# Kernel tuning notes

Hardware: AMD Instinct MI355X
Metric: run time of the kernel (lower is better)

Reference implementation:

```python
import jax, jax.numpy as jnp
import numpy as np

HEADS = 64
VOCAB = 5
EPS = 1e-5

def _layer_norm(x, g, b):
    mu = jnp.mean(x, axis=-1, keepdims=True)
    var = jnp.var(x, axis=-1, keepdims=True)
    return (x - mu) * jax.lax.rsqrt(var + EPS) * g + b

def setup_inputs() -> dict:
    key = jax.random.key(0)
    ks = jax.random.split(key, 12)
    h = HEADS
    s = 1.0 / np.sqrt(h)
    return {
        "x": jax.random.normal(ks[0], (8, 384, 384, h), dtype=jnp.float32),
        "W1": jax.random.normal(ks[1], (h, h), dtype=jnp.float32) * s,
        "b1": jnp.zeros((h,), jnp.float32),
        "W2": jax.random.normal(ks[2], (h, h), dtype=jnp.float32) * s,
        "b2": jnp.zeros((h,), jnp.float32),
        "W3": jax.random.normal(ks[3], (h, h), dtype=jnp.float32) * s,
        "b3": jnp.zeros((h,), jnp.float32),
        "ln_g": jnp.ones((h,), jnp.float32),
        "ln_b": jnp.zeros((h,), jnp.float32),
        "Wo": jax.random.normal(ks[4], (h, VOCAB), dtype=jnp.float32) * s,
        "bo": jnp.zeros((VOCAB,), jnp.float32),
    }

def reference(x, W1, b1, W2, b2, W3, b3, ln_g, ln_b, Wo, bo):
    # three (Linear -> gelu -> shared LayerNorm) blocks on [b,s,s,h]
    h = _layer_norm(jax.nn.gelu(x @ W1 + b1, approximate=False), ln_g, ln_b)
    h = _layer_norm(jax.nn.gelu(h @ W2 + b2, approximate=False), ln_g, ln_b)
    h = _layer_norm(jax.nn.gelu(h @ W3 + b3, approximate=False), ln_g, ln_b)
    out = h @ Wo + bo  # [b,s,s,vocab]
    return (out + jnp.swapaxes(out, 1, 2)) * 0.5
```

## Files before the change

### kernel.cpp

```cpp
#include <hip/hip_runtime.h>
#include <cstdint>
#include <cstddef>

typedef __attribute__((ext_vector_type(8))) __bf16   bf16x8;
typedef __attribute__((ext_vector_type(2))) __bf16   bf16x2;
typedef __attribute__((ext_vector_type(4))) float    f32x4;
typedef __attribute__((ext_vector_type(4))) uint32_t u32x4;

#define SDIM     384
#define VOCAB    5
#define SPW      8
#define WGPB     288
#define BLOCKS   (8 * WGPB)

#define WO_OFF   24576
#define BIAS_OFF 26624
#define OUT_OFF  27392

__device__ __forceinline__ f32x4 gelu4(f32x4 x){
  f32x4 u = x * x;
  f32x4 w = u * (-0.10294456f) + (-2.3021255f);
  f32x4 z = x * w;
  f32x4 e;
  e[0] = __builtin_amdgcn_exp2f(z[0]);
  e[1] = __builtin_amdgcn_exp2f(z[1]);
  e[2] = __builtin_amdgcn_exp2f(z[2]);
  e[3] = __builtin_amdgcn_exp2f(z[3]);
  f32x4 d = e + 1.0f;
  f32x4 r;
  r[0] = __builtin_amdgcn_rcpf(d[0]);
  r[1] = __builtin_amdgcn_rcpf(d[1]);
  r[2] = __builtin_amdgcn_rcpf(d[2]);
  r[3] = __builtin_amdgcn_rcpf(d[3]);
  return x * r;
}

__device__ __forceinline__ bf16x8 mk_bf8(f32x4 a, f32x4 b){
  bf16x8 v;
  v[0]=(__bf16)a[0]; v[1]=(__bf16)a[1]; v[2]=(__bf16)a[2]; v[3]=(__bf16)a[3];
  v[4]=(__bf16)b[0]; v[5]=(__bf16)b[1]; v[6]=(__bf16)b[2]; v[7]=(__bf16)b[3];
  return v;
}

__device__ __forceinline__ int perm_rho(int m){
  return (m & 0x23) | ((m & 4) << 2) | ((m & 0x18) >> 1);
}

__global__ __launch_bounds__(256)
void mlp_sym_kernel(const float* __restrict__ x,
                    const float* __restrict__ W1, const float* __restrict__ b1,
                    const float* __restrict__ W2, const float* __restrict__ b2,
                    const float* __restrict__ W3, const float* __restrict__ b3,
                    const float* __restrict__ lng, const float* __restrict__ lnb,
                    const float* __restrict__ Wo,  const float* __restrict__ bo,
                    float* __restrict__ out)
{
  __shared__ __align__(16) uint8_t Wl[37632];

  const int tid = threadIdx.x;

  {
    int m = tid & 63, g = tid >> 6;
    int rho = perm_rho(m);
    uint8_t* wrow = Wl + rho * 128;
    int swz = (rho & 7) << 4;
    #pragma unroll 1
    for (int idx = g; idx < 96; idx += 4) {
      int L = idx >> 5, kp = idx & 31;
      const float* W = (L == 0) ? W1 : ((L == 1) ? W2 : W3);
      float lo = W[(2 * kp    ) * 64 + m];
      float hi = W[(2 * kp + 1) * 64 + m];
      bf16x2 p = { (__bf16)lo, (__bf16)hi };
      *(uint32_t*)(wrow + L * 8192 + ((4 * kp) ^ swz)) = __builtin_bit_cast(uint32_t, p);
    }
    int mm = tid & 15;
    #pragma unroll 1
    for (int kp = tid >> 4; kp < 32; kp += 16) {
      float lo = (mm < VOCAB) ? Wo[(2 * kp    ) * VOCAB + mm] : 0.0f;
      float hi = (mm < VOCAB) ? Wo[(2 * kp + 1) * VOCAB + mm] : 0.0f;
      bf16x2 p = { (__bf16)lo, (__bf16)hi };
      *(uint32_t*)(Wl + WO_OFF + mm * 128 + ((4 * kp) ^ ((mm & 7) << 4))) =
          __builtin_bit_cast(uint32_t, p);
    }
    if (tid < 192) {
      float v = (tid < 64) ? b1[tid] : ((tid < 128) ? b2[tid - 64] : b3[tid - 128]);
      *(float*)(Wl + BIAS_OFF + tid * 4) = v;
    }
  }
  __syncthreads();

  const int bb  = blockIdx.x / WGPB;
  const int rem = blockIdx.x - bb * WGPB;
  int I0, J0, I1, J1;
  bool diag;
  if (rem < 276) {
    int I = 0, acc = 0;
    while (acc + (23 - I) <= rem) { acc += 23 - I; ++I; }
    int J = I + 1 + (rem - acc);
    I0 = I << 4; J0 = J << 4; I1 = J << 4; J1 = I << 4; diag = false;
  } else {
    int d = rem - 276;
    I0 = J0 = (2 * d) << 4; I1 = J1 = (2 * d + 1) << 4; diag = true;
  }

  const int wav  = tid >> 6, lane = tid & 63;
  const int h    = lane >> 4;
  const int b    = lane & 15;
  const int swzW = (b & 7) << 4;
  const int rowB = b * 128;
  const int kOff = 16 * h;
  const float* biasL = (const float*)(Wl + BIAS_OFF);
  float* outS = (float*)(Wl + OUT_OFF);

  const int blk  = wav >> 1, half = wav & 1;
  const int rowb = (blk ? I1 : I0) + 8 * half;
  const int colb = (blk ? J1 : J0);
  const long base0 = ((long)(bb * SDIM + rowb)) * SDIM + colb;

  f32x4 ggr[4], bbr[4], aoInit;
  #pragma unroll
  for (int mt = 0; mt < 4; ++mt) {
    int base = 8 * h + 4 * (mt & 1) + 32 * (mt >> 1);
    ggr[mt] = *(const f32x4*)(lng + base);
    bbr[mt] = *(const f32x4*)(lnb + base);
  }
  #pragma unroll
  for (int r = 0; r < 4; ++r) {
    int v = 4 * h + r;
    aoInit[r] = (v < VOCAB) ? bo[v] : 0.0f;
  }

  f32x4 xn[4];
  {
    const float* px = x + (size_t)(base0 + b) * 64 + 8 * h;
    xn[0] = *(const f32x4*)(px);      xn[1] = *(const f32x4*)(px + 4);
    xn[2] = *(const f32x4*)(px + 32); xn[3] = *(const f32x4*)(px + 36);
  }

  #pragma unroll 1
  for (int i = 0; i < SPW; ++i) {
    u32x4 bfr[2];
    bfr[0] = __builtin_bit_cast(u32x4, mk_bf8(xn[0], xn[1]));
    bfr[1] = __builtin_bit_cast(u32x4, mk_bf8(xn[2], xn[3]));

    {
      int inext = (i + 1 < SPW) ? (i + 1) : i;
      const float* pn = x + (size_t)(base0 + inext * SDIM + b) * 64 + 8 * h;
      xn[0] = *(const f32x4*)(pn);      xn[1] = *(const f32x4*)(pn + 4);
      xn[2] = *(const f32x4*)(pn + 32); xn[3] = *(const f32x4*)(pn + 36);
    }

    #pragma unroll
    for (int L = 0; L < 3; ++L) {
      const uint8_t* wp = Wl + L * 8192 + rowB;
      f32x4 acc[4];
      #pragma unroll
      for (int mt = 0; mt < 4; ++mt) {
        u32x4 w0 = *(const u32x4*)(wp + mt * 2048 + ((kOff     ) ^ swzW));
        u32x4 w1 = *(const u32x4*)(wp + mt * 2048 + ((kOff + 64) ^ swzW));
        int base = 8 * h + 4 * (mt & 1) + 32 * (mt >> 1);
        acc[mt] = *(const f32x4*)(biasL + L * 64 + base);
        acc[mt] = __builtin_amdgcn_mfma_f32_16x16x32_bf16(
            __builtin_bit_cast(bf16x8, w0), __builtin_bit_cast(bf16x8, bfr[0]), acc[mt], 0, 0, 0);
        acc[mt] = __builtin_amdgcn_mfma_f32_16x16x32_bf16(
            __builtin_bit_cast(bf16x8, w1), __builtin_bit_cast(bf16x8, bfr[1]), acc[mt], 0, 0, 0);
      }

      #pragma unroll
      for (int mt = 0; mt < 4; ++mt) acc[mt] = gelu4(acc[mt]);

      f32x4 vs = acc[0] + acc[1] + acc[2] + acc[3];
      f32x4 vq = acc[0]*acc[0] + acc[1]*acc[1] + acc[2]*acc[2] + acc[3]*acc[3];
      float s1 = (vs[0]+vs[1]) + (vs[2]+vs[3]);
      float s2 = (vq[0]+vq[1]) + (vq[2]+vq[3]);
      s1 += __shfl_xor(s1, 16); s2 += __shfl_xor(s2, 16);
      s1 += __shfl_xor(s1, 32); s2 += __shfl_xor(s2, 32);
      float mu   = s1 * (1.0f/64.0f);
      float var  = __builtin_fmaf(s2, (1.0f/64.0f), -mu * mu);
      float rstd = rsqrtf(var + 1e-5f);
      float nm   = -mu * rstd;

      f32x4 n0 = (acc[0] * rstd + nm) * ggr[0] + bbr[0];
      f32x4 n1 = (acc[1] * rstd + nm) * ggr[1] + bbr[1];
      f32x4 n2 = (acc[2] * rstd + nm) * ggr[2] + bbr[2];
      f32x4 n3 = (acc[3] * rstd + nm) * ggr[3] + bbr[3];
      bfr[0] = __builtin_bit_cast(u32x4, mk_bf8(n0, n1));
      bfr[1] = __builtin_bit_cast(u32x4, mk_bf8(n2, n3));
    }

    f32x4 ao = aoInit;
    {
      const uint8_t* wp = Wl + WO_OFF + rowB;
      u32x4 w0 = *(const u32x4*)(wp + ((kOff     ) ^ swzW));
      u32x4 w1 = *(const u32x4*)(wp + ((kOff + 64) ^ swzW));
      ao = __builtin_amdgcn_mfma_f32_16x16x32_bf16(
          __builtin_bit_cast(bf16x8, w0), __builtin_bit_cast(bf16x8, bfr[0]), ao, 0, 0, 0);
      ao = __builtin_amdgcn_mfma_f32_16x16x32_bf16(
          __builtin_bit_cast(bf16x8, w1), __builtin_bit_cast(bf16x8, bfr[1]), ao, 0, 0, 0);
    }

    float* myF = outS + blk * 1280 + (8 * half + i) * 80;
    #pragma unroll
    for (int r = 0; r < 4; ++r) {
      int v = 4 * h + r;
      if (v < VOCAB) myF[b * VOCAB + v] = ao[r];
    }
  }
  __syncthreads();

  #pragma unroll 1
  for (int idx = tid; idx < 2560; idx += 256) {
    int bk = (idx >= 1280) ? 1 : 0;
    int q2 = idx - bk * 1280;
    int r  = q2 / 80;
    int q  = q2 - r * 80;
    int c  = q / 5;
    int v  = q - c * 5;
    int pb = diag ? bk : 1 - bk;
    float val = 0.5f * (outS[bk * 1280 + r * 80 + q] +
                        outS[pb * 1280 + c * 80 + r * 5 + v]);
    int ii = (bk ? I1 : I0) + r;
    int jj = (bk ? J1 : J0) + c;
    out[((size_t)(bb * SDIM + ii) * SDIM + jj) * VOCAB + v] = val;
  }
}

extern "C" void kernel_launch(void* const* d_in, const int* in_sizes, int n_in,
                              void* d_out, int out_size, void* d_ws, size_t ws_size,
                              hipStream_t stream)
{
  const float* x   = (const float*)d_in[0];
  const float* W1  = (const float*)d_in[1];
  const float* b1  = (const float*)d_in[2];
  const float* W2  = (const float*)d_in[3];
  const float* b2  = (const float*)d_in[4];
  const float* W3  = (const float*)d_in[5];
  const float* b3  = (const float*)d_in[6];
  const float* lng = (const float*)d_in[7];
  const float* lnb = (const float*)d_in[8];
  const float* Wo  = (const float*)d_in[9];
  const float* bo  = (const float*)d_in[10];

  float* out = (float*)d_out;

  mlp_sym_kernel<<<BLOCKS, 256, 0, stream>>>(x, W1, b1, W2, b2, W3, b3,
                                             lng, lnb, Wo, bo, out);
}
```

Measured before the change: 136.8 us.

## Convert to persistent kernel with atomic work-stealing over tile units

The kernel now launches a fixed grid of 512 persistent blocks that fetch tile-pair units from a global atomic counter, instead of one block per unit. Weights are staged into LDS once per block rather than once per unit, and load balance is dynamic. The cost is an extra memset launch, an atomic per unit, and an extra barrier per unit. 512 blocks may also under-fill the device's CUs compared with the original 2304-block grid.

```diff
diff --git a/kernel.cpp b/kernel.cpp
--- a/kernel.cpp
+++ b/kernel.cpp
@@ -11,11 +11,13 @@
 #define VOCAB    5
 #define SPW      8
 #define WGPB     288
-#define BLOCKS   (8 * WGPB)
+#define UNITS    (8 * WGPB)
+#define PBLOCKS  512
 
 #define WO_OFF   24576
 #define BIAS_OFF 26624
 #define OUT_OFF  27392
+#define NU_OFF   37632
 
 __device__ __forceinline__ f32x4 gelu4(f32x4 x){
   f32x4 u = x * x;
@@ -46,53 +48,10 @@
   return (m & 0x23) | ((m & 4) << 2) | ((m & 0x18) >> 1);
 }
 
-__global__ __launch_bounds__(256)
-void mlp_sym_kernel(const float* __restrict__ x,
-                    const float* __restrict__ W1, const float* __restrict__ b1,
-                    const float* __restrict__ W2, const float* __restrict__ b2,
-                    const float* __restrict__ W3, const float* __restrict__ b3,
-                    const float* __restrict__ lng, const float* __restrict__ lnb,
-                    const float* __restrict__ Wo,  const float* __restrict__ bo,
-                    float* __restrict__ out)
-{
-  __shared__ __align__(16) uint8_t Wl[37632];
-
-  const int tid = threadIdx.x;
-
-  {
-    int m = tid & 63, g = tid >> 6;
-    int rho = perm_rho(m);
-    uint8_t* wrow = Wl + rho * 128;
-    int swz = (rho & 7) << 4;
-    #pragma unroll 1
-    for (int idx = g; idx < 96; idx += 4) {
-      int L = idx >> 5, kp = idx & 31;
-      const float* W = (L == 0) ? W1 : ((L == 1) ? W2 : W3);
-      float lo = W[(2 * kp    ) * 64 + m];
-      float hi = W[(2 * kp + 1) * 64 + m];
-      bf16x2 p = { (__bf16)lo, (__bf16)hi };
-      *(uint32_t*)(wrow + L * 8192 + ((4 * kp) ^ swz)) = __builtin_bit_cast(uint32_t, p);
-    }
-    int mm = tid & 15;
-    #pragma unroll 1
-    for (int kp = tid >> 4; kp < 32; kp += 16) {
-      float lo = (mm < VOCAB) ? Wo[(2 * kp    ) * VOCAB + mm] : 0.0f;
-      float hi = (mm < VOCAB) ? Wo[(2 * kp + 1) * VOCAB + mm] : 0.0f;
-      bf16x2 p = { (__bf16)lo, (__bf16)hi };
-      *(uint32_t*)(Wl + WO_OFF + mm * 128 + ((4 * kp) ^ ((mm & 7) << 4))) =
-          __builtin_bit_cast(uint32_t, p);
-    }
-    if (tid < 192) {
-      float v = (tid < 64) ? b1[tid] : ((tid < 128) ? b2[tid - 64] : b3[tid - 128]);
-      *(float*)(Wl + BIAS_OFF + tid * 4) = v;
-    }
-  }
-  __syncthreads();
-
-  const int bb  = blockIdx.x / WGPB;
-  const int rem = blockIdx.x - bb * WGPB;
-  int I0, J0, I1, J1;
-  bool diag;
+__device__ __forceinline__ void decode_unit(int u, int& bb, int& I0, int& J0,
+                                            int& I1, int& J1, bool& diag){
+  bb = u / WGPB;
+  int rem = u - bb * WGPB;
   if (rem < 276) {
     int I = 0, acc = 0;
     while (acc + (23 - I) <= rem) { acc += 23 - I; ++I; }
@@ -102,6 +61,50 @@
     int d = rem - 276;
     I0 = J0 = (2 * d) << 4; I1 = J1 = (2 * d + 1) << 4; diag = true;
   }
+}
+
+__global__ __launch_bounds__(256)
+void mlp_sym_kernel(const float* __restrict__ x,
+                    const float* __restrict__ W1, const float* __restrict__ b1,
+                    const float* __restrict__ W2, const float* __restrict__ b2,
+                    const float* __restrict__ W3, const float* __restrict__ b3,
+                    const float* __restrict__ lng, const float* __restrict__ lnb,
+                    const float* __restrict__ Wo,  const float* __restrict__ bo,
+                    float* __restrict__ out, unsigned int* __restrict__ counter)
+{
+  __shared__ __align__(16) uint8_t Wl[37696];
+
+  const int tid = threadIdx.x;
+
+  {
+    int m = tid & 63, g = tid >> 6;
+    int rho = perm_rho(m);
+    uint8_t* wrow = Wl + rho * 128;
+    int swz = (rho & 7) << 4;
+    #pragma unroll 1
+    for (int idx = g; idx < 96; idx += 4) {
+      int L = idx >> 5, kp = idx & 31;
+      const float* W = (L == 0) ? W1 : ((L == 1) ? W2 : W3);
+      float lo = W[(2 * kp    ) * 64 + m];
+      float hi = W[(2 * kp + 1) * 64 + m];
+      bf16x2 p = { (__bf16)lo, (__bf16)hi };
+      *(uint32_t*)(wrow + L * 8192 + ((4 * kp) ^ swz)) = __builtin_bit_cast(uint32_t, p);
+    }
+    int mm = tid & 15;
+    #pragma unroll 1
+    for (int kp = tid >> 4; kp < 32; kp += 16) {
+      float lo = (mm < VOCAB) ? Wo[(2 * kp    ) * VOCAB + mm] : 0.0f;
+      float hi = (mm < VOCAB) ? Wo[(2 * kp + 1) * VOCAB + mm] : 0.0f;
+      bf16x2 p = { (__bf16)lo, (__bf16)hi };
+      *(uint32_t*)(Wl + WO_OFF + mm * 128 + ((4 * kp) ^ ((mm & 7) << 4))) =
+          __builtin_bit_cast(uint32_t, p);
+    }
+    if (tid < 192) {
+      float v = (tid < 64) ? b1[tid] : ((tid < 128) ? b2[tid - 64] : b3[tid - 128]);
+      *(float*)(Wl + BIAS_OFF + tid * 4) = v;
+    }
+  }
+  __syncthreads();
 
   const int wav  = tid >> 6, lane = tid & 63;
   const int h    = lane >> 4;
@@ -111,11 +114,8 @@
   const int kOff = 16 * h;
   const float* biasL = (const float*)(Wl + BIAS_OFF);
   float* outS = (float*)(Wl + OUT_OFF);
-
+  volatile int* nuS = (volatile int*)(Wl + NU_OFF);
   const int blk  = wav >> 1, half = wav & 1;
-  const int rowb = (blk ? I1 : I0) + 8 * half;
-  const int colb = (blk ? J1 : J0);
-  const long base0 = ((long)(bb * SDIM + rowb)) * SDIM + colb;
 
   f32x4 ggr[4], bbr[4], aoInit;
   #pragma unroll
@@ -130,98 +130,115 @@
     aoInit[r] = (v < VOCAB) ? bo[v] : 0.0f;
   }
 
-  f32x4 xn[4];
-  {
-    const float* px = x + (size_t)(base0 + b) * 64 + 8 * h;
-    xn[0] = *(const f32x4*)(px);      xn[1] = *(const f32x4*)(px + 4);
-    xn[2] = *(const f32x4*)(px + 32); xn[3] = *(const f32x4*)(px + 36);
-  }
-
-  #pragma unroll 1
-  for (int i = 0; i < SPW; ++i) {
-    u32x4 bfr[2];
-    bfr[0] = __builtin_bit_cast(u32x4, mk_bf8(xn[0], xn[1]));
-    bfr[1] = __builtin_bit_cast(u32x4, mk_bf8(xn[2], xn[3]));
-
+  int u = blockIdx.x;
+
+  while (u < UNITS) {
+    int bb, I0, J0, I1, J1; bool diag;
+    decode_unit(u, bb, I0, J0, I1, J1, diag);
+
+    const int rowb = (blk ? I1 : I0) + 8 * half;
+    const int colb = (blk ? J1 : J0);
+    const long base0 = ((long)(bb * SDIM + rowb)) * SDIM + colb;
+
+    f32x4 xn[4];
     {
-      int inext = (i + 1 < SPW) ? (i + 1) : i;
-      const float* pn = x + (size_t)(base0 + inext * SDIM + b) * 64 + 8 * h;
-      xn[0] = *(const f32x4*)(pn);      xn[1] = *(const f32x4*)(pn + 4);
-      xn[2] = *(const f32x4*)(pn + 32); xn[3] = *(const f32x4*)(pn + 36);
-    }
-
-    #pragma unroll
-    for (int L = 0; L < 3; ++L) {
-      const uint8_t* wp = Wl + L * 8192 + rowB;
-      f32x4 acc[4];
+      const float* px = x + (size_t)(base0 + b) * 64 + 8 * h;
+      xn[0] = *(const f32x4*)(px);      xn[1] = *(const f32x4*)(px + 4);
+      xn[2] = *(const f32x4*)(px + 32); xn[3] = *(const f32x4*)(px + 36);
+    }
+
+    #pragma unroll 1
+    for (int i = 0; i < SPW; ++i) {
+      u32x4 bfr[2];
+      bfr[0] = __builtin_bit_cast(u32x4, mk_bf8(xn[0], xn[1]));
+      bfr[1] = __builtin_bit_cast(u32x4, mk_bf8(xn[2], xn[3]));
+
+      {
+        int inext = (i + 1 < SPW) ? (i + 1) : i;
+        const float* pn = x + (size_t)(base0 + inext * SDIM + b) * 64 + 8 * h;
+        xn[0] = *(const f32x4*)(pn);      xn[1] = *(const f32x4*)(pn + 4);
+        xn[2] = *(const f32x4*)(pn + 32); xn[3] = *(const f32x4*)(pn + 36);
+      }
+
       #pragma unroll
-      for (int mt = 0; mt < 4; ++mt) {
-        u32x4 w0 = *(const u32x4*)(wp + mt * 2048 + ((kOff     ) ^ swzW));
-        u32x4 w1 = *(const u32x4*)(wp + mt * 2048 + ((kOff + 64) ^ swzW));
-        int base = 8 * h + 4 * (mt & 1) + 32 * (mt >> 1);
-        acc[mt] = *(const f32x4*)(biasL + L * 64 + base);
-        acc[mt] = __builtin_amdgcn_mfma_f32_16x16x32_bf16(
-            __builtin_bit_cast(bf16x8, w0), __builtin_bit_cast(bf16x8, bfr[0]), acc[mt], 0, 0, 0);
-        acc[mt] = __builtin_amdgcn_mfma_f32_16x16x32_bf16(
-            __builtin_bit_cast(bf16x8, w1), __builtin_bit_cast(bf16x8, bfr[1]), acc[mt], 0, 0, 0);
-      }
-
+      for (int L = 0; L < 3; ++L) {
+        const uint8_t* wp = Wl + L * 8192 + rowB;
+        f32x4 acc[4];
+        #pragma unroll
+        for (int mt = 0; mt < 4; ++mt) {
+          u32x4 w0 = *(const u32x4*)(wp + mt * 2048 + ((kOff     ) ^ swzW));
+          u32x4 w1 = *(const u32x4*)(wp + mt * 2048 + ((kOff + 64) ^ swzW));
+          int base = 8 * h + 4 * (mt & 1) + 32 * (mt >> 1);
+          acc[mt] = *(const f32x4*)(biasL + L * 64 + base);
+          acc[mt] = __builtin_amdgcn_mfma_f32_16x16x32_bf16(
+              __builtin_bit_cast(bf16x8, w0), __builtin_bit_cast(bf16x8, bfr[0]), acc[mt], 0, 0, 0);
+          acc[mt] = __builtin_amdgcn_mfma_f32_16x16x32_bf16(
+              __builtin_bit_cast(bf16x8, w1), __builtin_bit_cast(bf16x8, bfr[1]), acc[mt], 0, 0, 0);
+        }
+
+        #pragma unroll
+        for (int mt = 0; mt < 4; ++mt) acc[mt] = gelu4(acc[mt]);
+
+        f32x4 vs = acc[0] + acc[1] + acc[2] + acc[3];
+        f32x4 vq = acc[0]*acc[0] + acc[1]*acc[1] + acc[2]*acc[2] + acc[3]*acc[3];
+        float s1 = (vs[0]+vs[1]) + (vs[2]+vs[3]);
+        float s2 = (vq[0]+vq[1]) + (vq[2]+vq[3]);
+        s1 += __shfl_xor(s1, 16); s2 += __shfl_xor(s2, 16);
+        s1 += __shfl_xor(s1, 32); s2 += __shfl_xor(s2, 32);
+        float mu   = s1 * (1.0f/64.0f);
+        float var  = __builtin_fmaf(s2, (1.0f/64.0f), -mu * mu);
+        float rstd = rsqrtf(var + 1e-5f);
+        float nm   = -mu * rstd;
+
+        f32x4 n0 = (acc[0] * rstd + nm) * ggr[0] + bbr[0];
+        f32x4 n1 = (acc[1] * rstd + nm) * ggr[1] + bbr[1];
+        f32x4 n2 = (acc[2] * rstd + nm) * ggr[2] + bbr[2];
+        f32x4 n3 = (acc[3] * rstd + nm) * ggr[3] + bbr[3];
+        bfr[0] = __builtin_bit_cast(u32x4, mk_bf8(n0, n1));
+        bfr[1] = __builtin_bit_cast(u32x4, mk_bf8(n2, n3));
+      }
+
+      f32x4 ao = aoInit;
+      {
+        const uint8_t* wp = Wl + WO_OFF + rowB;
+        u32x4 w0 = *(const u32x4*)(wp + ((kOff     ) ^ swzW));
+        u32x4 w1 = *(const u32x4*)(wp + ((kOff + 64) ^ swzW));
+        ao = __builtin_amdgcn_mfma_f32_16x16x32_bf16(
+            __builtin_bit_cast(bf16x8, w0), __builtin_bit_cast(bf16x8, bfr[0]), ao, 0, 0, 0);
+        ao = __builtin_amdgcn_mfma_f32_16x16x32_bf16(
+            __builtin_bit_cast(bf16x8, w1), __builtin_bit_cast(bf16x8, bfr[1]), ao, 0, 0, 0);
+      }
+
+      float* myF = outS + blk * 1280 + (8 * half + i) * 80;
       #pragma unroll
-      for (int mt = 0; mt < 4; ++mt) acc[mt] = gelu4(acc[mt]);
-
-      f32x4 vs = acc[0] + acc[1] + acc[2] + acc[3];
-      f32x4 vq = acc[0]*acc[0] + acc[1]*acc[1] + acc[2]*acc[2] + acc[3]*acc[3];
-      float s1 = (vs[0]+vs[1]) + (vs[2]+vs[3]);
-      float s2 = (vq[0]+vq[1]) + (vq[2]+vq[3]);
-      s1 += __shfl_xor(s1, 16); s2 += __shfl_xor(s2, 16);
-      s1 += __shfl_xor(s1, 32); s2 += __shfl_xor(s2, 32);
-      float mu   = s1 * (1.0f/64.0f);
-      float var  = __builtin_fmaf(s2, (1.0f/64.0f), -mu * mu);
-      float rstd = rsqrtf(var + 1e-5f);
-      float nm   = -mu * rstd;
-
-      f32x4 n0 = (acc[0] * rstd + nm) * ggr[0] + bbr[0];
-      f32x4 n1 = (acc[1] * rstd + nm) * ggr[1] + bbr[1];
-      f32x4 n2 = (acc[2] * rstd + nm) * ggr[2] + bbr[2];
-      f32x4 n3 = (acc[3] * rstd + nm) * ggr[3] + bbr[3];
-      bfr[0] = __builtin_bit_cast(u32x4, mk_bf8(n0, n1));
-      bfr[1] = __builtin_bit_cast(u32x4, mk_bf8(n2, n3));
-    }
-
-    f32x4 ao = aoInit;
-    {
-      const uint8_t* wp = Wl + WO_OFF + rowB;
-      u32x4 w0 = *(const u32x4*)(wp + ((kOff     ) ^ swzW));
-      u32x4 w1 = *(const u32x4*)(wp + ((kOff + 64) ^ swzW));
-      ao = __builtin_amdgcn_mfma_f32_16x16x32_bf16(
-          __builtin_bit_cast(bf16x8, w0), __builtin_bit_cast(bf16x8, bfr[0]), ao, 0, 0, 0);
-      ao = __builtin_amdgcn_mfma_f32_16x16x32_bf16(
-          __builtin_bit_cast(bf16x8, w1), __builtin_bit_cast(bf16x8, bfr[1]), ao, 0, 0, 0);
-    }
-
-    float* myF = outS + blk * 1280 + (8 * half + i) * 80;
-    #pragma unroll
-    for (int r = 0; r < 4; ++r) {
-      int v = 4 * h + r;
-      if (v < VOCAB) myF[b * VOCAB + v] = ao[r];
-    }
-  }
-  __syncthreads();
-
-  #pragma unroll 1
-  for (int idx = tid; idx < 2560; idx += 256) {
-    int bk = (idx >= 1280) ? 1 : 0;
-    int q2 = idx - bk * 1280;
-    int r  = q2 / 80;
-    int q  = q2 - r * 80;
-    int c  = q / 5;
-    int v  = q - c * 5;
-    int pb = diag ? bk : 1 - bk;
-    float val = 0.5f * (outS[bk * 1280 + r * 80 + q] +
-                        outS[pb * 1280 + c * 80 + r * 5 + v]);
-    int ii = (bk ? I1 : I0) + r;
-    int jj = (bk ? J1 : J0) + c;
-    out[((size_t)(bb * SDIM + ii) * SDIM + jj) * VOCAB + v] = val;
+      for (int r = 0; r < 4; ++r) {
+        int v = 4 * h + r;
+        if (v < VOCAB) myF[b * VOCAB + v] = ao[r];
+      }
+    }
+
+    if (tid == 0) *nuS = PBLOCKS + (int)atomicAdd(counter, 1u);
+    __syncthreads();
+    int un = *nuS;
+
+    #pragma unroll 1
+    for (int idx = tid; idx < 2560; idx += 256) {
+      int bk = (idx >= 1280) ? 1 : 0;
+      int q2 = idx - bk * 1280;
+      int r  = q2 / 80;
+      int q  = q2 - r * 80;
+      int c  = q / 5;
+      int v  = q - c * 5;
+      int pb = diag ? bk : 1 - bk;
+      float val = 0.5f * (outS[bk * 1280 + r * 80 + q] +
+                          outS[pb * 1280 + c * 80 + r * 5 + v]);
+      int ii = (bk ? I1 : I0) + r;
+      int jj = (bk ? J1 : J0) + c;
+      out[((size_t)(bb * SDIM + ii) * SDIM + jj) * VOCAB + v] = val;
+    }
+    __syncthreads();
+
+    u = un;
   }
 }
 
@@ -242,7 +259,10 @@
   const float* bo  = (const float*)d_in[10];
 
   float* out = (float*)d_out;
-
-  mlp_sym_kernel<<<BLOCKS, 256, 0, stream>>>(x, W1, b1, W2, b2, W3, b3,
-                                             lng, lnb, Wo, bo, out);
-}
+  unsigned int* counter = (unsigned int*)d_ws;
+
+  hipMemsetAsync(counter, 0, sizeof(unsigned int), stream);
+
+  mlp_sym_kernel<<<PBLOCKS, 256, 0, stream>>>(x, W1, b1, W2, b2, W3, b3,
+                                              lng, lnb, Wo, bo, out, counter);
+}
```

Result: no change. 136.7 us (-0.1%).
